# Optimization experiments

Measured on AMD Instinct MI355X. Metric: run time of the kernel, lower is better.

Reference implementation:

```python
import jax, jax.numpy as jnp
import numpy as np

IN_C = 128
OUT_C = 128
N_SAMPLES = 9
N_HEADS = 8
HEAD_C = OUT_C // N_HEADS
SCALE = HEAD_C ** (-0.5)
B, FH, FW = 4, 128, 128


def setup_inputs() -> dict:
    key = jax.random.key(0)
    ks = jax.random.split(key, 8)
    w_std = IN_C ** (-0.5)
    q = jax.random.normal(ks[0], (B, IN_C, FH, FW), dtype=jnp.float32)
    kv = jax.random.normal(ks[1], (B, IN_C, N_SAMPLES, FH * FW), dtype=jnp.float32)
    Wq = jax.random.normal(ks[2], (OUT_C, IN_C), dtype=jnp.float32) * w_std
    bq = jax.random.normal(ks[3], (OUT_C,), dtype=jnp.float32) * 0.01
    Wk = jax.random.normal(ks[4], (OUT_C, IN_C), dtype=jnp.float32) * w_std
    bk = jax.random.normal(ks[5], (OUT_C,), dtype=jnp.float32) * 0.01
    Wv = jax.random.normal(ks[6], (OUT_C, IN_C), dtype=jnp.float32) * w_std
    bv = jax.random.normal(ks[7], (OUT_C,), dtype=jnp.float32) * 0.01
    return {"q": q, "kv": kv, "Wq": Wq, "bq": bq, "Wk": Wk, "bk": bk, "Wv": Wv, "bv": bv}


def reference(q, kv, Wq, bq, Wk, bk, Wv, bv):
    b, c, fh, fw = q.shape
    d = fh * fw
    # 1x1 conv projections == channel matmuls
    qp = (jnp.einsum('oc,bchw->bohw', Wq, q) + bq[None, :, None, None])
    qp = qp.reshape(b * N_HEADS, HEAD_C, d)                       # [bH, hc, d]
    kp = (jnp.einsum('oc,bcsd->bosd', Wk, kv) + bk[None, :, None, None])
    kp = kp.reshape(b * N_HEADS, HEAD_C, N_SAMPLES, d)            # [bH, hc, s, d]
    vp = (jnp.einsum('oc,bcsd->bosd', Wv, kv) + bv[None, :, None, None])
    vp = vp.reshape(b * N_HEADS, HEAD_C, N_SAMPLES, d)
    # per-pixel attention over n_samples keys
    attn = jnp.einsum('bcd,bcsd->bsd', qp, kp) * SCALE            # [bH, s, d]
    attn = jax.nn.softmax(attn, axis=1)
    out = jnp.einsum('bsd,bcsd->bcd', attn, vp)                   # [bH, hc, d]
    return out.reshape(b, OUT_C, fh, fw)
```

## Files before the change

kernel.cpp:

```cpp
#include <hip/hip_runtime.h>

#define D_PIX 16384
#define NSMP  9
#define TP    64
#define RS    136

typedef __attribute__((ext_vector_type(8))) short s16x8;
typedef __attribute__((ext_vector_type(4))) short s16x4;
typedef __attribute__((ext_vector_type(4))) float f32x4;

__device__ __forceinline__ short f2b(float f) {
    union { float f; unsigned u; } c; c.f = f;
    unsigned r = (c.u + 0x7FFFu + ((c.u >> 16) & 1u)) >> 16;
    return (short)r;
}

__global__ __launch_bounds__(256, 2)
void deform_attn_kernel(const float* __restrict__ q,
                        const float* __restrict__ kv,
                        const float* __restrict__ Wq,
                        const float* __restrict__ bq,
                        const float* __restrict__ Wk,
                        const float* __restrict__ bk,
                        const float* __restrict__ Wv,
                        const float* __restrict__ bv,
                        float* __restrict__ out)
{
    __shared__ short ldsb[2][TP * RS];

    const int tid  = threadIdx.x;
    const int bid  = blockIdx.x;
    const int b    = bid >> 8;
    const int px0  = (bid & 255) * TP;
    const int lane = tid & 63;
    const int w    = tid >> 6;
    const int r    = lane & 15;
    const int quad = lane >> 4;

    const int pxb = (tid & 7) * 8;
    const int chb = (tid >> 3) * 4;

    f32x4 pref[4][2];
    auto stage_load = [&](const float* base, int chstride) {
        #pragma unroll
        for (int j = 0; j < 4; ++j) {
            const float* p = base + (long)(chb + j) * chstride + pxb;
            pref[j][0] = *(const f32x4*)p;
            pref[j][1] = *(const f32x4*)(p + 4);
        }
    };
    auto stage_write = [&](short* buf) {
        #pragma unroll
        for (int i = 0; i < 8; ++i) {
            s16x4 v4 = { f2b(pref[0][i >> 2][i & 3]), f2b(pref[1][i >> 2][i & 3]),
                         f2b(pref[2][i >> 2][i & 3]), f2b(pref[3][i >> 2][i & 3]) };
            *(s16x4*)(buf + (pxb + i) * RS + chb) = v4;
        }
    };
    auto load_bfrags = [&](const short* buf, int n, s16x8* bfr) {
        #pragma unroll
        for (int ks = 0; ks < 4; ++ks)
            bfr[ks] = *(const s16x8*)(buf + (n * 16 + r) * RS + ks * 32 + quad * 8);
    };
    auto load_wfrag = [&](const float* W, int o, int ks) -> s16x8 {
        const float* p = W + o * 128 + ks * 32 + quad * 8;
        f32x4 a = *(const f32x4*)p;
        f32x4 c = *(const f32x4*)(p + 4);
        s16x8 f = { f2b(a[0]), f2b(a[1]), f2b(a[2]), f2b(a[3]),
                    f2b(c[0]), f2b(c[1]), f2b(c[2]), f2b(c[3]) };
        return f;
    };

    s16x8 wkF[2][4], wvF[2][4];
    float bkf[2][4], bvf[2][4], bqf[2][4];
    #pragma unroll
    for (int m = 0; m < 2; ++m) {
        const int o = (2 * w + m) * 16 + r;
        #pragma unroll
        for (int ks = 0; ks < 4; ++ks) {
            wkF[m][ks] = load_wfrag(Wk, o, ks);
            wvF[m][ks] = load_wfrag(Wv, o, ks);
        }
        const int ob = (2 * w + m) * 16 + quad * 4;
        #pragma unroll
        for (int rr = 0; rr < 4; ++rr) {
            bqf[m][rr] = bq[ob + rr];
            bkf[m][rr] = bk[ob + rr];
            bvf[m][rr] = bv[ob + rr];
        }
    }

    float qp[2][4][4];
    float oacc[2][4][4];
    float lsum[2][4];
    #pragma unroll
    for (int m = 0; m < 2; ++m)
        #pragma unroll
        for (int n = 0; n < 4; ++n) {
            lsum[m][n] = 0.f;
            #pragma unroll
            for (int rr = 0; rr < 4; ++rr) oacc[m][n][rr] = 0.f;
        }

    const float* qbase  = q  + (long)(b * 128) * D_PIX + px0;
    const float* kvbase = kv + (long)(b * 128) * NSMP * D_PIX + px0;

    stage_load(qbase, D_PIX);
    stage_write(ldsb[0]);
    __syncthreads();

    stage_load(kvbase, NSMP * D_PIX);
    {
        s16x8 wqF[2][4];
        #pragma unroll
        for (int m = 0; m < 2; ++m) {
            const int o = (2 * w + m) * 16 + r;
            #pragma unroll
            for (int ks = 0; ks < 4; ++ks)
                wqF[m][ks] = load_wfrag(Wq, o, ks);
        }
        #pragma unroll
        for (int n = 0; n < 4; ++n) {
            s16x8 bfr[4];
            load_bfrags(ldsb[0], n, bfr);
            #pragma unroll
            for (int m = 0; m < 2; ++m) {
                f32x4 acc = {0.f, 0.f, 0.f, 0.f};
                #pragma unroll
                for (int ks = 0; ks < 4; ++ks)
                    acc = __builtin_amdgcn_mfma_f32_16x16x32_bf16(wqF[m][ks], bfr[ks], acc, 0, 0, 0);
                #pragma unroll
                for (int rr = 0; rr < 4; ++rr) qp[m][n][rr] = acc[rr] + bqf[m][rr];
            }
        }
    }
    stage_write(ldsb[1]);
    __syncthreads();

    for (int s = 0; s < NSMP; ++s) {
        if (s < NSMP - 1) stage_load(kvbase + (s + 1) * D_PIX, NSMP * D_PIX);
        const short* buf = ldsb[(s + 1) & 1];
        #pragma unroll
        for (int n = 0; n < 4; ++n) {
            s16x8 bfr[4];
            load_bfrags(buf, n, bfr);
            #pragma unroll
            for (int m = 0; m < 2; ++m) {
                f32x4 kacc = {0.f, 0.f, 0.f, 0.f};
                f32x4 vacc = {0.f, 0.f, 0.f, 0.f};
                #pragma unroll
                for (int ks = 0; ks < 4; ++ks) {
                    kacc = __builtin_amdgcn_mfma_f32_16x16x32_bf16(wkF[m][ks], bfr[ks], kacc, 0, 0, 0);
                    vacc = __builtin_amdgcn_mfma_f32_16x16x32_bf16(wvF[m][ks], bfr[ks], vacc, 0, 0, 0);
                }
                float pf = 0.f;
                #pragma unroll
                for (int rr = 0; rr < 4; ++rr) pf += qp[m][n][rr] * (kacc[rr] + bkf[m][rr]);
                pf += __shfl_xor(pf, 16, 64);
                pf += __shfl_xor(pf, 32, 64);
                const float e = __expf(pf * 0.25f);
                lsum[m][n] += e;
                #pragma unroll
                for (int rr = 0; rr < 4; ++rr) oacc[m][n][rr] += e * (vacc[rr] + bvf[m][rr]);
            }
        }
        if (s < NSMP - 1) stage_write(ldsb[s & 1]);
        __syncthreads();
    }

    #pragma unroll
    for (int m = 0; m < 2; ++m) {
        #pragma unroll
        for (int n = 0; n < 4; ++n) {
            const float inv = 1.f / lsum[m][n];
            #pragma unroll
            for (int rr = 0; rr < 4; ++rr) {
                const int o = (2 * w + m) * 16 + quad * 4 + rr;
                out[(long)(b * 128 + o) * D_PIX + px0 + n * 16 + r] = oacc[m][n][rr] * inv;
            }
        }
    }
}

extern "C" void kernel_launch(void* const* d_in, const int* in_sizes, int n_in,
                              void* d_out, int out_size, void* d_ws, size_t ws_size,
                              hipStream_t stream) {
    const float* q  = (const float*)d_in[0];
    const float* kv = (const float*)d_in[1];
    const float* Wq = (const float*)d_in[2];
    const float* bq = (const float*)d_in[3];
    const float* Wk = (const float*)d_in[4];
    const float* bk = (const float*)d_in[5];
    const float* Wv = (const float*)d_in[6];
    const float* bv = (const float*)d_in[7];
    float* out = (float*)d_out;

    dim3 grid(1024);
    dim3 block(256);
    hipLaunchKernelGGL(deform_attn_kernel, grid, block, 0, stream,
                       q, kv, Wq, bq, Wk, bk, Wv, bv, out);
}
```

Baseline: 457.0 us.

## Switch to 32x32x16 MFMA tiles, fold biases algebraically, swizzle LDS, use packed bf16 convert

```diff
diff --git a/kernel.cpp b/kernel.cpp
--- a/kernel.cpp
+++ b/kernel.cpp
@@ -5,14 +5,18 @@
 #define TP    64
 #define RS    136
 
-typedef __attribute__((ext_vector_type(8))) short s16x8;
-typedef __attribute__((ext_vector_type(4))) short s16x4;
-typedef __attribute__((ext_vector_type(4))) float f32x4;
-
-__device__ __forceinline__ short f2b(float f) {
-    union { float f; unsigned u; } c; c.f = f;
-    unsigned r = (c.u + 0x7FFFu + ((c.u >> 16) & 1u)) >> 16;
-    return (short)r;
+typedef __attribute__((ext_vector_type(8)))  short s16x8;
+typedef __attribute__((ext_vector_type(4)))  float f32x4;
+typedef __attribute__((ext_vector_type(16))) float f32x16;
+
+__device__ __forceinline__ int cvt2(float lo, float hi) {
+    int r;
+    asm("v_cvt_pk_bf16_f32 %0, %1, %2" : "=v"(r) : "v"(lo), "v"(hi));
+    return r;
+}
+
+__device__ __forceinline__ int swz(int row, int col) {
+    return col ^ (((row >> 3) & 3) << 3);
 }
 
 __global__ __launch_bounds__(256, 2)
@@ -34,11 +38,13 @@
     const int px0  = (bid & 255) * TP;
     const int lane = tid & 63;
     const int w    = tid >> 6;
-    const int r    = lane & 15;
-    const int quad = lane >> 4;
+    const int cl   = lane & 31;
+    const int hi   = lane >> 5;
+    const int wch  = w * 32;
 
     const int pxb = (tid & 7) * 8;
     const int chb = (tid >> 3) * 4;
+    const int swr = ((tid & 7) & 3) << 3;
 
     f32x4 pref[4][2];
     auto stage_load = [&](const float* base, int chstride) {
@@ -52,55 +58,43 @@
     auto stage_write = [&](short* buf) {
         #pragma unroll
         for (int i = 0; i < 8; ++i) {
-            s16x4 v4 = { f2b(pref[0][i >> 2][i & 3]), f2b(pref[1][i >> 2][i & 3]),
-                         f2b(pref[2][i >> 2][i & 3]), f2b(pref[3][i >> 2][i & 3]) };
-            *(s16x4*)(buf + (pxb + i) * RS + chb) = v4;
-        }
-    };
-    auto load_bfrags = [&](const short* buf, int n, s16x8* bfr) {
-        #pragma unroll
-        for (int ks = 0; ks < 4; ++ks)
-            bfr[ks] = *(const s16x8*)(buf + (n * 16 + r) * RS + ks * 32 + quad * 8);
-    };
-    auto load_wfrag = [&](const float* W, int o, int ks) -> s16x8 {
-        const float* p = W + o * 128 + ks * 32 + quad * 8;
+            int2 v;
+            v.x = cvt2(pref[0][i >> 2][i & 3], pref[1][i >> 2][i & 3]);
+            v.y = cvt2(pref[2][i >> 2][i & 3], pref[3][i >> 2][i & 3]);
+            *(int2*)(buf + (pxb + i) * RS + (chb ^ swr)) = v;
+        }
+    };
+    auto ldb = [&](const short* buf, int n, int ks) -> s16x8 {
+        const int row = n * 32 + cl;
+        const int col = ks * 16 + hi * 8;
+        return *(const s16x8*)(buf + row * RS + swz(row, col));
+    };
+    auto ldw = [&](const float* W, int ks) -> s16x8 {
+        const float* p = W + (wch + cl) * 128 + ks * 16 + hi * 8;
         f32x4 a = *(const f32x4*)p;
         f32x4 c = *(const f32x4*)(p + 4);
-        s16x8 f = { f2b(a[0]), f2b(a[1]), f2b(a[2]), f2b(a[3]),
-                    f2b(c[0]), f2b(c[1]), f2b(c[2]), f2b(c[3]) };
-        return f;
-    };
-
-    s16x8 wkF[2][4], wvF[2][4];
-    float bkf[2][4], bvf[2][4], bqf[2][4];
+        union { s16x8 v; int i[4]; } u;
+        u.i[0] = cvt2(a[0], a[1]); u.i[1] = cvt2(a[2], a[3]);
+        u.i[2] = cvt2(c[0], c[1]); u.i[3] = cvt2(c[2], c[3]);
+        return u.v;
+    };
+
+    s16x8 wkF[8], wvF[8];
     #pragma unroll
-    for (int m = 0; m < 2; ++m) {
-        const int o = (2 * w + m) * 16 + r;
-        #pragma unroll
-        for (int ks = 0; ks < 4; ++ks) {
-            wkF[m][ks] = load_wfrag(Wk, o, ks);
-            wvF[m][ks] = load_wfrag(Wv, o, ks);
-        }
-        const int ob = (2 * w + m) * 16 + quad * 4;
-        #pragma unroll
-        for (int rr = 0; rr < 4; ++rr) {
-            bqf[m][rr] = bq[ob + rr];
-            bkf[m][rr] = bk[ob + rr];
-            bvf[m][rr] = bv[ob + rr];
-        }
-    }
-
-    float qp[2][4][4];
-    float oacc[2][4][4];
-    float lsum[2][4];
+    for (int ks = 0; ks < 8; ++ks) { wkF[ks] = ldw(Wk, ks); wvF[ks] = ldw(Wv, ks); }
+
+    float bkv[16], bqv[16];
     #pragma unroll
-    for (int m = 0; m < 2; ++m)
-        #pragma unroll
-        for (int n = 0; n < 4; ++n) {
-            lsum[m][n] = 0.f;
-            #pragma unroll
-            for (int rr = 0; rr < 4; ++rr) oacc[m][n][rr] = 0.f;
-        }
+    for (int r = 0; r < 16; ++r) {
+        const int o = wch + (r & 3) + 8 * (r >> 2) + 4 * hi;
+        bkv[r] = bk[o];
+        bqv[r] = bq[o];
+    }
+
+    float qp[2][16];
+    float oacc[2][16];
+    float ls[2][2];
+    float qb4[2][2];
 
     const float* qbase  = q  + (long)(b * 128) * D_PIX + px0;
     const float* kvbase = kv + (long)(b * 128) * NSMP * D_PIX + px0;
@@ -111,73 +105,79 @@
 
     stage_load(kvbase, NSMP * D_PIX);
     {
-        s16x8 wqF[2][4];
-        #pragma unroll
-        for (int m = 0; m < 2; ++m) {
-            const int o = (2 * w + m) * 16 + r;
-            #pragma unroll
-            for (int ks = 0; ks < 4; ++ks)
-                wqF[m][ks] = load_wfrag(Wq, o, ks);
-        }
-        #pragma unroll
-        for (int n = 0; n < 4; ++n) {
-            s16x8 bfr[4];
-            load_bfrags(ldsb[0], n, bfr);
-            #pragma unroll
-            for (int m = 0; m < 2; ++m) {
-                f32x4 acc = {0.f, 0.f, 0.f, 0.f};
-                #pragma unroll
-                for (int ks = 0; ks < 4; ++ks)
-                    acc = __builtin_amdgcn_mfma_f32_16x16x32_bf16(wqF[m][ks], bfr[ks], acc, 0, 0, 0);
-                #pragma unroll
-                for (int rr = 0; rr < 4; ++rr) qp[m][n][rr] = acc[rr] + bqf[m][rr];
+        s16x8 wqF[8];
+        #pragma unroll
+        for (int ks = 0; ks < 8; ++ks) wqF[ks] = ldw(Wq, ks);
+        #pragma unroll
+        for (int n = 0; n < 2; ++n) {
+            f32x16 acc;
+            #pragma unroll
+            for (int r = 0; r < 16; ++r) acc[r] = 0.f;
+            #pragma unroll
+            for (int ks = 0; ks < 8; ++ks)
+                acc = __builtin_amdgcn_mfma_f32_32x32x16_bf16(wqF[ks], ldb(ldsb[0], n, ks), acc, 0, 0, 0);
+            float t0 = 0.f, t1 = 0.f;
+            #pragma unroll
+            for (int r = 0; r < 16; ++r) {
+                const float v = acc[r] + bqv[r];
+                qp[n][r] = v;
+                if (r < 8) t0 += v * bkv[r]; else t1 += v * bkv[r];
             }
+            t0 += __shfl_xor(t0, 32);
+            t1 += __shfl_xor(t1, 32);
+            qb4[n][0] = t0 * 0.25f;
+            qb4[n][1] = t1 * 0.25f;
+            ls[n][0] = ls[n][1] = 0.f;
+            #pragma unroll
+            for (int r = 0; r < 16; ++r) oacc[n][r] = 0.f;
         }
     }
     stage_write(ldsb[1]);
     __syncthreads();
 
     for (int s = 0; s < NSMP; ++s) {
-        if (s < NSMP - 1) stage_load(kvbase + (s + 1) * D_PIX, NSMP * D_PIX);
+        if (s < NSMP - 1) stage_load(kvbase + (long)(s + 1) * D_PIX, NSMP * D_PIX);
         const short* buf = ldsb[(s + 1) & 1];
         #pragma unroll
-        for (int n = 0; n < 4; ++n) {
-            s16x8 bfr[4];
-            load_bfrags(buf, n, bfr);
-            #pragma unroll
-            for (int m = 0; m < 2; ++m) {
-                f32x4 kacc = {0.f, 0.f, 0.f, 0.f};
-                f32x4 vacc = {0.f, 0.f, 0.f, 0.f};
-                #pragma unroll
-                for (int ks = 0; ks < 4; ++ks) {
-                    kacc = __builtin_amdgcn_mfma_f32_16x16x32_bf16(wkF[m][ks], bfr[ks], kacc, 0, 0, 0);
-                    vacc = __builtin_amdgcn_mfma_f32_16x16x32_bf16(wvF[m][ks], bfr[ks], vacc, 0, 0, 0);
-                }
-                float pf = 0.f;
-                #pragma unroll
-                for (int rr = 0; rr < 4; ++rr) pf += qp[m][n][rr] * (kacc[rr] + bkf[m][rr]);
-                pf += __shfl_xor(pf, 16, 64);
-                pf += __shfl_xor(pf, 32, 64);
-                const float e = __expf(pf * 0.25f);
-                lsum[m][n] += e;
-                #pragma unroll
-                for (int rr = 0; rr < 4; ++rr) oacc[m][n][rr] += e * (vacc[rr] + bvf[m][rr]);
+        for (int n = 0; n < 2; ++n) {
+            f32x16 kacc, vacc;
+            #pragma unroll
+            for (int r = 0; r < 16; ++r) { kacc[r] = 0.f; vacc[r] = 0.f; }
+            #pragma unroll
+            for (int ks = 0; ks < 8; ++ks) {
+                const s16x8 bfr = ldb(buf, n, ks);
+                kacc = __builtin_amdgcn_mfma_f32_32x32x16_bf16(wkF[ks], bfr, kacc, 0, 0, 0);
+                vacc = __builtin_amdgcn_mfma_f32_32x32x16_bf16(wvF[ks], bfr, vacc, 0, 0, 0);
             }
+            float p0 = 0.f, p1 = 0.f;
+            #pragma unroll
+            for (int r = 0; r < 8; ++r)  p0 += qp[n][r] * kacc[r];
+            #pragma unroll
+            for (int r = 8; r < 16; ++r) p1 += qp[n][r] * kacc[r];
+            p0 += __shfl_xor(p0, 32);
+            p1 += __shfl_xor(p1, 32);
+            const float e0 = __expf(fmaf(p0, 0.25f, qb4[n][0]));
+            const float e1 = __expf(fmaf(p1, 0.25f, qb4[n][1]));
+            ls[n][0] += e0;
+            ls[n][1] += e1;
+            #pragma unroll
+            for (int r = 0; r < 8; ++r)  oacc[n][r] += e0 * vacc[r];
+            #pragma unroll
+            for (int r = 8; r < 16; ++r) oacc[n][r] += e1 * vacc[r];
         }
         if (s < NSMP - 1) stage_write(ldsb[s & 1]);
         __syncthreads();
     }
 
     #pragma unroll
-    for (int m = 0; m < 2; ++m) {
-        #pragma unroll
-        for (int n = 0; n < 4; ++n) {
-            const float inv = 1.f / lsum[m][n];
-            #pragma unroll
-            for (int rr = 0; rr < 4; ++rr) {
-                const int o = (2 * w + m) * 16 + quad * 4 + rr;
-                out[(long)(b * 128 + o) * D_PIX + px0 + n * 16 + r] = oacc[m][n][rr] * inv;
-            }
+    for (int n = 0; n < 2; ++n) {
+        const float i0 = 1.f / ls[n][0];
+        const float i1 = 1.f / ls[n][1];
+        #pragma unroll
+        for (int r = 0; r < 16; ++r) {
+            const int o = wch + (r & 3) + 8 * (r >> 2) + 4 * hi;
+            out[(long)(b * 128 + o) * D_PIX + px0 + n * 32 + cl] =
+                oacc[n][r] * (r < 8 ? i0 : i1) + bv[o];
         }
     }
 }
```

Result: slower. 466.9 us (+2.2%).
